# Kernel optimization log

Measured on AMD Instinct MI355X. Metric: run time of the kernel, lower is better.

## Reference

```python
import jax, jax.numpy as jnp
import numpy as np

N = 50000
EPS = 1e-5

def gcn_conv(x, W, b, edge_index):
    # PyG GCNConv: transform first, then normalized aggregation with self-loops
    xw = x @ W  # [N, out]
    src = jnp.concatenate([edge_index[0], jnp.arange(N)])  # add self-loops
    dst = jnp.concatenate([edge_index[1], jnp.arange(N)])
    deg = jax.ops.segment_sum(jnp.ones_like(dst, dtype=xw.dtype), dst, num_segments=N)
    dis = jnp.where(deg > 0, deg ** -0.5, 0.0)
    norm = dis[src] * dis[dst]  # [E+N]
    out = jax.ops.segment_sum(norm[:, None] * xw[src], dst, num_segments=N)
    return out + b

def batchnorm(x, gamma, beta):
    mean = x.mean(axis=0)
    var = ((x - mean) ** 2).mean(axis=0)  # biased var (training mode)
    return gamma * (x - mean) * jax.lax.rsqrt(var + EPS) + beta

def lrelu(x):
    return jnp.where(x > 0, x, 0.1 * x)

def setup_inputs() -> dict:
    key = jax.random.key(0)
    ks = jax.random.split(key, 12)
    E = 800000
    d = {
        "x": jax.random.normal(ks[0], (N, 3), dtype=jnp.float32),
        "edge_index": jax.random.randint(ks[1], (2, E), 0, N),
        "W1": jax.random.normal(ks[2], (3, 64), dtype=jnp.float32) * (1.0 / np.sqrt(3)),
        "b1": jnp.zeros((64,), jnp.float32),
        "g1": jnp.ones((64,), jnp.float32),
        "be1": jnp.zeros((64,), jnp.float32),
        "W2": jax.random.normal(ks[3], (64, 64), dtype=jnp.float32) * 0.125,
        "b2": jnp.zeros((64,), jnp.float32),
        "g2": jnp.ones((64,), jnp.float32),
        "be2": jnp.zeros((64,), jnp.float32),
        "W3": jax.random.normal(ks[4], (64, 256), dtype=jnp.float32) * 0.125,
        "b3": jnp.zeros((256,), jnp.float32),
        "g3": jnp.ones((256,), jnp.float32),
        "be3": jnp.zeros((256,), jnp.float32),
        "W4": jax.random.normal(ks[5], (256, 1), dtype=jnp.float32) * (1.0 / 16.0),
        "b4": jnp.zeros((1,), jnp.float32),
    }
    return d

def reference(x, edge_index, W1, b1, g1, be1, W2, b2, g2, be2, W3, b3, g3, be3, W4, b4):
    h = lrelu(batchnorm(gcn_conv(x, W1, b1, edge_index), g1, be1))
    h = lrelu(batchnorm(gcn_conv(h, W2, b2, edge_index), g2, be2))
    h = lrelu(batchnorm(gcn_conv(h, W3, b3, edge_index), g3, be3))
    h = gcn_conv(h, W4, b4, edge_index)
    return jax.nn.sigmoid(h)
```

## Files before the change

kernel.cpp:

```cpp
#include <hip/hip_runtime.h>
#include <math.h>

#define NN 50000
#define NP 50048
#define NB (NP / 64)
#define SCAN_NB ((NN + 255) / 256)
#define NBKT ((NN + 255) / 256)

typedef unsigned short u16;
typedef unsigned int u32;

typedef __bf16 bf16x8 __attribute__((ext_vector_type(8)));
typedef float f32x4 __attribute__((ext_vector_type(4)));

__device__ __forceinline__ u16 f2bf(float f) {
    u32 u = __float_as_uint(f);
    u32 r = (u + 0x7FFFu + ((u >> 16) & 1u)) >> 16;
    return (u16)r;
}
__device__ __forceinline__ float bf2f_lo(u32 v) { return __uint_as_float(v << 16); }
__device__ __forceinline__ float bf2f_hi(u32 v) { return __uint_as_float(v & 0xFFFF0000u); }

__global__ __launch_bounds__(256) void k_binA(const int* __restrict__ dst, int E,
                                              int* __restrict__ bcntT, int nblk) {
    __shared__ int h[NBKT];
    for (int i = threadIdx.x; i < NBKT; i += 256) h[i] = 0;
    __syncthreads();
    int base = blockIdx.x * 4096;
#pragma unroll
    for (int i = 0; i < 16; i++) {
        int e = base + i * 256 + threadIdx.x;
        if (e < E) atomicAdd(&h[dst[e] >> 8], 1);
    }
    __syncthreads();
    for (int i = threadIdx.x; i < NBKT; i += 256) bcntT[i * nblk + blockIdx.x] = h[i];
}

__global__ __launch_bounds__(256) void k_binT(const int* __restrict__ bcntT,
        int* __restrict__ colpre, int* __restrict__ tot, int nblk) {
    __shared__ int sh[256];
    int k = blockIdx.x, t = threadIdx.x;
    int v = (t < nblk) ? bcntT[k * nblk + t] : 0;
    sh[t] = v; __syncthreads();
    int inc = v;
    for (int o = 1; o < 256; o <<= 1) {
        int p = (t >= o) ? sh[t - o] : 0;
        __syncthreads();
        inc += p; sh[t] = inc;
        __syncthreads();
    }
    if (t < nblk) colpre[k * nblk + t] = inc - v;
    if (t == 255) tot[k] = inc;
}

__global__ __launch_bounds__(256) void k_scan_tot(const int* __restrict__ tot,
                                                  int* __restrict__ bstart, int E) {
    __shared__ int sh[256];
    int t = threadIdx.x;
    int v = (t < NBKT) ? tot[t] : 0;
    sh[t] = v; __syncthreads();
    int inc = v;
    for (int o = 1; o < 256; o <<= 1) {
        int p = (t >= o) ? sh[t - o] : 0;
        __syncthreads();
        inc += p; sh[t] = inc;
        __syncthreads();
    }
    if (t < NBKT) bstart[t] = inc - v;
    if (t == NBKT - 1) bstart[NBKT] = E;
}

__global__ __launch_bounds__(256) void k_binB(const int* __restrict__ src,
        const int* __restrict__ dst, int E, const int* __restrict__ bstart,
        const int* __restrict__ colpre, int nblk, u32* __restrict__ ebuf) {
    __shared__ int h[NBKT];
    __shared__ int base[NBKT];
    int b = blockIdx.x;
    for (int i = threadIdx.x; i < NBKT; i += 256) {
        h[i] = 0;
        base[i] = bstart[i] + colpre[i * nblk + b];
    }
    __syncthreads();
    int bb = b * 4096;
#pragma unroll
    for (int i = 0; i < 16; i++) {
        int e = bb + i * 256 + threadIdx.x;
        if (e < E) {
            int d = dst[e];
            int k = d >> 8;
            int r = atomicAdd(&h[k], 1);
            ebuf[base[k] + r] = ((u32)d << 16) | (u32)src[e];
        }
    }
}

__global__ __launch_bounds__(256) void k_bcnt_bsum_dis(const u32* __restrict__ ebuf,
        const int* __restrict__ bstart, int* __restrict__ cnt, float* __restrict__ dis,
        int* __restrict__ bsum, int n) {
    __shared__ int h[256];
    __shared__ int red[256];
    int k = blockIdx.x, t = threadIdx.x;
    h[t] = 0; __syncthreads();
    int beg = bstart[k], end = bstart[k + 1];
    for (int j = beg + t; j < end; j += 256)
        atomicAdd(&h[(ebuf[j] >> 16) & 255], 1);
    __syncthreads();
    int r = k * 256 + t;
    int d = h[t];
    bool valid = (r < n);
    if (valid) { cnt[r] = d; dis[r] = rsqrtf((float)d + 1.0f); }
    red[t] = valid ? d : 0;
    __syncthreads();
    for (int off = 128; off; off >>= 1) {
        if (t < off) red[t] += red[t + off];
        __syncthreads();
    }
    if (t == 0) bsum[k] = red[0];
}

__global__ void k_scan_bsum(int* __restrict__ bsum, int nb) {
    __shared__ int sh[256];
    int t = threadIdx.x;
    int v0 = (t < nb) ? bsum[t] : 0;
    sh[t] = v0; __syncthreads();
    int inc = v0;
    for (int off = 1; off < 256; off <<= 1) {
        int o = (t >= off) ? sh[t - off] : 0;
        __syncthreads();
        inc += o; sh[t] = inc;
        __syncthreads();
    }
    if (t < nb) bsum[t] = inc - v0;
}

__global__ __launch_bounds__(256) void k_sfpb(const int* __restrict__ cnt,
        const int* __restrict__ bpre, int* __restrict__ rowstart,
        const float* __restrict__ x, const float* __restrict__ dis,
        float* __restrict__ p0, const u32* __restrict__ ebuf,
        const int* __restrict__ bstart, u16* __restrict__ adj, int n, int E) {
    __shared__ int sh[256];
    __shared__ int cur[256];
    int b = blockIdx.x, t = threadIdx.x;
    int i = b * 256 + t;
    int v0 = (i < n) ? cnt[i] : 0;
    sh[t] = v0; __syncthreads();
    int inc = v0;
    for (int off = 1; off < 256; off <<= 1) {
        int o = (t >= off) ? sh[t - off] : 0;
        __syncthreads();
        inc += o; sh[t] = inc;
        __syncthreads();
    }
    int rs = bpre[b] + inc - v0;
    if (i < n) {
        rowstart[i] = rs;
        float dv = dis[i];
        ((float4*)p0)[i] = make_float4(dv * x[i * 3], dv * x[i * 3 + 1], dv * x[i * 3 + 2], 0.f);
    }
    if (b == gridDim.x - 1 && t == 0) rowstart[n] = E;
    cur[t] = rs;
    __syncthreads();
    int beg = bstart[b], end = bstart[b + 1];
    for (int j = beg + t; j < end; j += 256) {
        u32 e = ebuf[j];
        int p = atomicAdd(&cur[(e >> 16) & 255], 1);
        adj[p] = (u16)(e & 0xFFFF);
    }
}

__global__ void k_wprep_all(const float* __restrict__ W2, const float* __restrict__ W3,
                            u16* __restrict__ w2h, u16* __restrict__ w2l,
                            u16* __restrict__ w3h, u16* __restrict__ w3l) {
    int idx = blockIdx.x * 256 + threadIdx.x;
    float w; u16* ph; u16* pl; int slot;
    if (idx < 64 * 64) {
        int o = idx >> 6, k = idx & 63;
        w = W2[k * 64 + o]; ph = w2h; pl = w2l; slot = o * 64 + k;
    } else if (idx < 64 * 64 + 256 * 64) {
        int i2 = idx - 64 * 64;
        int o = i2 >> 6, k = i2 & 63;
        w = W3[k * 256 + o]; ph = w3h; pl = w3l; slot = o * 64 + k;
    } else return;
    u16 h = f2bf(w);
    float hf = __uint_as_float((u32)h << 16);
    ph[slot] = h;
    pl[slot] = f2bf(w - hf);
}

__global__ void k_gather3(const int* __restrict__ rowstart, const u16* __restrict__ adj,
                          const float* __restrict__ p0, const float* __restrict__ dis,
                          float* __restrict__ z, int n) {
    int row = blockIdx.x * 256 + threadIdx.x;
    if (row >= n) return;
    const float4* P4 = (const float4*)p0;
    float4 v = P4[row];
    float a0 = v.x, a1 = v.y, a2 = v.z;
    int beg = rowstart[row], end = rowstart[row + 1];
    for (int j = beg; j < end; j++) {
        int s = (int)__builtin_nontemporal_load(adj + j);
        float4 w = P4[s];
        a0 += w.x; a1 += w.y; a2 += w.z;
    }
    float dv = dis[row];
    z[row * 3] = dv * a0; z[row * 3 + 1] = dv * a1; z[row * 3 + 2] = dv * a2;
}

__global__ __launch_bounds__(256) void k_gather64_bf16(const int* __restrict__ rowstart,
        const u16* __restrict__ adj, const u16* __restrict__ pb,
        const float* __restrict__ dis, u16* __restrict__ zb, int n) {
    int row = blockIdx.x * 16 + (threadIdx.x >> 4);
    int lane = threadIdx.x & 15;
    if (row >= n) return;
    uint2 v = *((const uint2*)(pb + ((size_t)row << 6)) + lane);
    float a0 = bf2f_lo(v.x), a1 = bf2f_hi(v.x), a2 = bf2f_lo(v.y), a3 = bf2f_hi(v.y);
    int beg = rowstart[row], end = rowstart[row + 1];
    int j = beg;
    for (; j + 3 < end; j += 4) {
        int s0 = (int)__builtin_nontemporal_load(adj + j);
        int s1 = (int)__builtin_nontemporal_load(adj + j + 1);
        int s2 = (int)__builtin_nontemporal_load(adj + j + 2);
        int s3 = (int)__builtin_nontemporal_load(adj + j + 3);
        uint2 v0 = *((const uint2*)(pb + ((size_t)s0 << 6)) + lane);
        uint2 v1 = *((const uint2*)(pb + ((size_t)s1 << 6)) + lane);
        uint2 v2 = *((const uint2*)(pb + ((size_t)s2 << 6)) + lane);
        uint2 v3 = *((const uint2*)(pb + ((size_t)s3 << 6)) + lane);
        a0 += (bf2f_lo(v0.x) + bf2f_lo(v1.x)) + (bf2f_lo(v2.x) + bf2f_lo(v3.x));
        a1 += (bf2f_hi(v0.x) + bf2f_hi(v1.x)) + (bf2f_hi(v2.x) + bf2f_hi(v3.x));
        a2 += (bf2f_lo(v0.y) + bf2f_lo(v1.y)) + (bf2f_lo(v2.y) + bf2f_lo(v3.y));
        a3 += (bf2f_hi(v0.y) + bf2f_hi(v1.y)) + (bf2f_hi(v2.y) + bf2f_hi(v3.y));
    }
    for (; j < end; j++) {
        int s = (int)__builtin_nontemporal_load(adj + j);
        uint2 v0 = *((const uint2*)(pb + ((size_t)s << 6)) + lane);
        a0 += bf2f_lo(v0.x); a1 += bf2f_hi(v0.x);
        a2 += bf2f_lo(v0.y); a3 += bf2f_hi(v0.y);
    }
    float dv = dis[row];
    uint2 o;
    o.x = (u32)f2bf(a0 * dv) | ((u32)f2bf(a1 * dv) << 16);
    o.y = (u32)f2bf(a2 * dv) | ((u32)f2bf(a3 * dv) << 16);
    ((uint2*)(zb + ((size_t)row << 6)))[lane] = o;
}

__global__ void k_gather1_final(const int* __restrict__ rowstart, const u16* __restrict__ adj,
                                const float* __restrict__ q, const float* __restrict__ dis,
                                const float* __restrict__ b4, float* __restrict__ out, int n) {
    int row = blockIdx.x * 256 + threadIdx.x;
    if (row >= n) return;
    float acc = q[row];
    int beg = rowstart[row], end = rowstart[row + 1];
    for (int j = beg; j < end; j++)
        acc += q[(int)__builtin_nontemporal_load(adj + j)];
    float v = dis[row] * acc + b4[0];
    out[row] = 1.f / (1.f + expf(-v));
}

__global__ __launch_bounds__(256) void k_mgemm(const u16* __restrict__ zb,
        const u16* __restrict__ wth, const u16* __restrict__ wtl,
        u16* __restrict__ t, int tstride,
        double* __restrict__ pS, double* __restrict__ pQ) {
    const int wv = threadIdx.x >> 6, lane = threadIdx.x & 63;
    const int lc = lane & 15, lk = lane >> 4;
    const int r0 = blockIdx.x * 64;
    const int col = blockIdx.y * 64 + wv * 16 + lc;

    const bf16x8* wh = (const bf16x8*)(wth + (size_t)col * 64 + lk * 8);
    const bf16x8* wl = (const bf16x8*)(wtl + (size_t)col * 64 + lk * 8);
    bf16x8 bh0 = wh[0], bh1 = wh[4];
    bf16x8 bl0 = wl[0], bl1 = wl[4];

    f32x4 acc[4] = {};
#pragma unroll
    for (int rt = 0; rt < 4; rt++) {
        const bf16x8* ap = (const bf16x8*)(zb + (size_t)(r0 + rt * 16 + lc) * 64 + lk * 8);
        bf16x8 a0 = ap[0], a1 = ap[4];
        acc[rt] = __builtin_amdgcn_mfma_f32_16x16x32_bf16(a0, bh0, acc[rt], 0, 0, 0);
        acc[rt] = __builtin_amdgcn_mfma_f32_16x16x32_bf16(a1, bh1, acc[rt], 0, 0, 0);
        acc[rt] = __builtin_amdgcn_mfma_f32_16x16x32_bf16(a0, bl0, acc[rt], 0, 0, 0);
        acc[rt] = __builtin_amdgcn_mfma_f32_16x16x32_bf16(a1, bl1, acc[rt], 0, 0, 0);
    }
#pragma unroll
    for (int rt = 0; rt < 4; rt++) {
        int rowb = r0 + rt * 16 + lk * 4;
#pragma unroll
        for (int rg = 0; rg < 4; rg++)
            t[(size_t)(rowb + rg) * tstride + col] = f2bf(acc[rt][rg]);
    }
    float s = 0.f, q = 0.f;
#pragma unroll
    for (int rt = 0; rt < 4; rt++)
#pragma unroll
        for (int rg = 0; rg < 4; rg++) { float v = acc[rt][rg]; s += v; q += v * v; }
    s += __shfl_xor(s, 16); q += __shfl_xor(q, 16);
    s += __shfl_xor(s, 32); q += __shfl_xor(q, 32);
    if (lane < 16) {
        pS[(size_t)col * NB + blockIdx.x] = (double)s;
        pQ[(size_t)col * NB + blockIdx.x] = (double)q;
    }
}

__global__ __launch_bounds__(256) void k_gemm3_stats(const float* __restrict__ z,
        const float* __restrict__ W, u16* __restrict__ t,
        double* __restrict__ pS, double* __restrict__ pQ, int n) {
    __shared__ float sH[64 * 4];
    __shared__ float sW[3 * 64];
    __shared__ double red[2 * 16 * 64];
    const int tid = threadIdx.x;
    const int r0 = blockIdx.x * 64;
    for (int i = tid; i < 192; i += 256) {
        int r = i / 3, c = i - r * 3;
        sH[r * 4 + c] = (r0 + r < n) ? z[(size_t)(r0 + r) * 3 + c] : 0.f;
    }
    if (tid < 48) ((float4*)sW)[tid] = ((const float4*)W)[tid];
    __syncthreads();
    const int tx = tid & 15, ty = tid >> 4;
    float4 acc[4];
#pragma unroll
    for (int r = 0; r < 4; r++) acc[r] = make_float4(0.f, 0.f, 0.f, 0.f);
    const float4* sW4 = (const float4*)sW;
#pragma unroll
    for (int k = 0; k < 3; k++) {
        float4 wv = sW4[k * 16 + tx];
#pragma unroll
        for (int r = 0; r < 4; r++) {
            float hs = sH[(ty * 4 + r) * 4 + k];
            acc[r].x += hs * wv.x; acc[r].y += hs * wv.y;
            acc[r].z += hs * wv.z; acc[r].w += hs * wv.w;
        }
    }
#pragma unroll
    for (int r = 0; r < 4; r++) {
        int row = r0 + ty * 4 + r;
        if (row < n) {
            uint2 o;
            o.x = (u32)f2bf(acc[r].x) | ((u32)f2bf(acc[r].y) << 16);
            o.y = (u32)f2bf(acc[r].z) | ((u32)f2bf(acc[r].w) << 16);
            *(uint2*)&t[(size_t)row * 64 + tx * 4] = o;
        }
    }
    double* redS = red;
    double* redQ = red + 16 * 64;
    double s0 = 0, s1 = 0, s2 = 0, s3 = 0, q0 = 0, q1 = 0, q2 = 0, q3 = 0;
#pragma unroll
    for (int r = 0; r < 4; r++) {
        s0 += acc[r].x; q0 += (double)acc[r].x * acc[r].x;
        s1 += acc[r].y; q1 += (double)acc[r].y * acc[r].y;
        s2 += acc[r].z; q2 += (double)acc[r].z * acc[r].z;
        s3 += acc[r].w; q3 += (double)acc[r].w * acc[r].w;
    }
    int base = ty * 64 + tx * 4;
    redS[base + 0] = s0; redS[base + 1] = s1; redS[base + 2] = s2; redS[base + 3] = s3;
    redQ[base + 0] = q0; redQ[base + 1] = q1; redQ[base + 2] = q2; redQ[base + 3] = q3;
    __syncthreads();
    if (ty == 0) {
#pragma unroll
        for (int jj = 0; jj < 4; jj++) {
            int c = tx * 4 + jj;
            double S = 0, Q = 0;
            for (int g = 0; g < 16; g++) { S += redS[g * 64 + c]; Q += redQ[g * 64 + c]; }
            pS[(size_t)c * NB + blockIdx.x] = S;
            pQ[(size_t)c * NB + blockIdx.x] = Q;
        }
    }
}

template<int F>
__global__ __launch_bounds__(256) void k_stats_fin(const double* __restrict__ pS,
        const double* __restrict__ pQ, const float* __restrict__ g,
        const float* __restrict__ be, double* __restrict__ st, int n) {
    __shared__ double shS[256], shQ[256];
    int c = blockIdx.x, t = threadIdx.x;
    double s = 0, q = 0;
    for (int i = t; i < NB; i += 256) {
        s += pS[(size_t)c * NB + i];
        q += pQ[(size_t)c * NB + i];
    }
    shS[t] = s; shQ[t] = q;
    __syncthreads();
    for (int off = 128; off; off >>= 1) {
        if (t < off) { shS[t] += shS[t + off]; shQ[t] += shQ[t + off]; }
        __syncthreads();
    }
    if (t == 0) {
        double mean = shS[0] / n;
        double var = shQ[0] / n - mean * mean;
        if (var < 0.0) var = 0.0;
        double mult = (double)g[c] / sqrt(var + 1e-5);
        st[2 * F + c] = mult;
        st[3 * F + c] = (double)be[c] - mult * mean;
    }
}

__global__ void k_apply64(const u16* __restrict__ t, const float* __restrict__ dis,
                          const double* __restrict__ st, u16* __restrict__ p, int n) {
    int idx = blockIdx.x * 256 + threadIdx.x;
    if (idx >= n * 16) return;
    int row = idx >> 4, c = (idx & 15) * 4;
    uint2 v = ((const uint2*)t)[idx];
    float f0 = bf2f_lo(v.x), f1 = bf2f_hi(v.x), f2 = bf2f_lo(v.y), f3 = bf2f_hi(v.y);
    float m0 = (float)st[128 + c], m1 = (float)st[129 + c],
          m2 = (float)st[130 + c], m3 = (float)st[131 + c];
    float a0 = (float)st[192 + c], a1 = (float)st[193 + c],
          a2 = (float)st[194 + c], a3 = (float)st[195 + c];
    float r0 = m0 * f0 + a0; r0 = r0 > 0.f ? r0 : 0.1f * r0;
    float r1 = m1 * f1 + a1; r1 = r1 > 0.f ? r1 : 0.1f * r1;
    float r2 = m2 * f2 + a2; r2 = r2 > 0.f ? r2 : 0.1f * r2;
    float r3 = m3 * f3 + a3; r3 = r3 > 0.f ? r3 : 0.1f * r3;
    float dv = dis[row];
    uint2 o;
    o.x = (u32)f2bf(r0 * dv) | ((u32)f2bf(r1 * dv) << 16);
    o.y = (u32)f2bf(r2 * dv) | ((u32)f2bf(r3 * dv) << 16);
    ((uint2*)p)[idx] = o;
}

__global__ void k_apply3_dot(const u16* __restrict__ t, const double* __restrict__ st,
                             const float* __restrict__ dis, const float* __restrict__ W4,
                             float* __restrict__ q, int n) {
    int row = blockIdx.x * 4 + (threadIdx.x >> 6);
    int lane = threadIdx.x & 63;
    if (row >= n) return;
    uint2 v = ((const uint2*)t)[(size_t)row * 64 + lane];
    float f0 = bf2f_lo(v.x), f1 = bf2f_hi(v.x), f2 = bf2f_lo(v.y), f3 = bf2f_hi(v.y);
    int c = lane * 4;
    float m0 = (float)st[512 + c], m1 = (float)st[513 + c],
          m2 = (float)st[514 + c], m3 = (float)st[515 + c];
    float a0 = (float)st[768 + c], a1 = (float)st[769 + c],
          a2 = (float)st[770 + c], a3 = (float)st[771 + c];
    float b0 = m0 * f0 + a0; b0 = b0 > 0.f ? b0 : 0.1f * b0;
    float b1 = m1 * f1 + a1; b1 = b1 > 0.f ? b1 : 0.1f * b1;
    float b2 = m2 * f2 + a2; b2 = b2 > 0.f ? b2 : 0.1f * b2;
    float b3 = m3 * f3 + a3; b3 = b3 > 0.f ? b3 : 0.1f * b3;
    float4 w = ((const float4*)W4)[lane];
    float s = b0 * w.x + b1 * w.y + b2 * w.z + b3 * w.w;
#pragma unroll
    for (int off = 32; off; off >>= 1) s += __shfl_down(s, off);
    if (lane == 0) q[row] = dis[row] * s;
}

extern "C" void kernel_launch(void* const* d_in, const int* in_sizes, int n_in,
                              void* d_out, int out_size, void* d_ws, size_t ws_size,
                              hipStream_t stream) {
    const float* x  = (const float*)d_in[0];
    const int*   ei = (const int*)d_in[1];
    const int E = in_sizes[1] / 2;
    const int* src = ei;
    const int* dst = ei + E;
    const float* W1 = (const float*)d_in[2];
    const float* g1 = (const float*)d_in[4];
    const float* be1= (const float*)d_in[5];
    const float* W2 = (const float*)d_in[6];
    const float* g2 = (const float*)d_in[8];
    const float* be2= (const float*)d_in[9];
    const float* W3 = (const float*)d_in[10];
    const float* g3 = (const float*)d_in[12];
    const float* be3= (const float*)d_in[13];
    const float* W4 = (const float*)d_in[14];
    const float* b4 = (const float*)d_in[15];
    float* out = (float*)d_out;

    const int nblk = (E + 4095) / 4096;

    u16*   T    = (u16*)d_ws;
    u16*   P    = T + (size_t)NP * 256;
    u16*   Zb   = P + (size_t)NN * 64;
    u16*   Wt2h = Zb + (size_t)NP * 64;
    u16*   Wt2l = Wt2h + 64 * 64;
    u16*   Wt3h = Wt2l + 64 * 64;
    u16*   Wt3l = Wt3h + 256 * 64;
    double* st  = (double*)(Wt3l + 256 * 64);
    double *st0 = st, *st1 = st + 1024, *st2 = st + 2048;
    double* pS  = st + 3 * 1024;
    double* pQ  = pS + (size_t)256 * NB;
    float* Z3   = (float*)(pQ + (size_t)256 * NB);
    float* P0   = Z3 + NN * 3;
    float* Q    = P0 + NN * 4;
    float* dis  = Q + NN;
    int* cnt      = (int*)(dis + NN);
    int* rowstart = cnt + NN;
    u16* adj      = (u16*)(rowstart + NN + 8);
    int* bsum     = (int*)(adj + E + (E & 1));
    u32* ebuf     = (u32*)(bsum + SCAN_NB + 4);
    int* bcntT    = (int*)(ebuf + E);
    int* colpre   = bcntT + NBKT * nblk;
    int* tot      = colpre + NBKT * nblk;
    int* bstart   = tot + NBKT + 4;

    hipMemsetAsync(Zb + (size_t)NN * 64, 0, (size_t)(NP - NN) * 64 * sizeof(u16), stream);

    k_binA<<<nblk, 256, 0, stream>>>(dst, E, bcntT, nblk);
    k_binT<<<NBKT, 256, 0, stream>>>(bcntT, colpre, tot, nblk);
    k_scan_tot<<<1, 256, 0, stream>>>(tot, bstart, E);
    k_binB<<<nblk, 256, 0, stream>>>(src, dst, E, bstart, colpre, nblk, ebuf);
    k_bcnt_bsum_dis<<<NBKT, 256, 0, stream>>>(ebuf, bstart, cnt, dis, bsum, NN);
    k_scan_bsum<<<1, 256, 0, stream>>>(bsum, SCAN_NB);
    k_sfpb<<<SCAN_NB, 256, 0, stream>>>(cnt, bsum, rowstart, x, dis, P0, ebuf, bstart,
                                        adj, NN, E);
    k_wprep_all<<<(64 * 64 + 256 * 64 + 255) / 256, 256, 0, stream>>>(W2, W3, Wt2h, Wt2l, Wt3h, Wt3l);

    const int rows_grid = (NN + 255) / 256;
    const int g16_grid  = (NN + 15) / 16;
    const int wave4_grid = (NN + 3) / 4;
    const int app_grid = (NN * 16 + 255) / 256;

    k_gather3<<<rows_grid, 256, 0, stream>>>(rowstart, adj, P0, dis, Z3, NN);
    k_gemm3_stats<<<NB, 256, 0, stream>>>(Z3, W1, T, pS, pQ, NN);
    k_stats_fin<64><<<64, 256, 0, stream>>>(pS, pQ, g1, be1, st0, NN);
    k_apply64<<<app_grid, 256, 0, stream>>>(T, dis, st0, P, NN);

    k_gather64_bf16<<<g16_grid, 256, 0, stream>>>(rowstart, adj, P, dis, Zb, NN);
    k_mgemm<<<dim3(NB, 1), 256, 0, stream>>>(Zb, Wt2h, Wt2l, T, 64, pS, pQ);
    k_stats_fin<64><<<64, 256, 0, stream>>>(pS, pQ, g2, be2, st1, NN);
    k_apply64<<<app_grid, 256, 0, stream>>>(T, dis, st1, P, NN);

    k_gather64_bf16<<<g16_grid, 256, 0, stream>>>(rowstart, adj, P, dis, Zb, NN);
    k_mgemm<<<dim3(NB, 4), 256, 0, stream>>>(Zb, Wt3h, Wt3l, T, 256, pS, pQ);
    k_stats_fin<256><<<256, 256, 0, stream>>>(pS, pQ, g3, be3, st2, NN);

    k_apply3_dot<<<wave4_grid, 256, 0, stream>>>(T, st2, dis, W4, Q, NN);
    k_gather1_final<<<rows_grid, 256, 0, stream>>>(rowstart, adj, Q, dis, b4, out, NN);
}
```

Baseline: 195.0 us.

## Fuse batchnorm+leaky-relu apply into neighbor gather and merge weight prep into binning

Removes the separate apply kernels. The gather kernel now reads raw pre-BN bf16 features and applies the BN affine transform, leaky ReLU and source-degree scaling to each neighbor on the fly. The weight-prep kernel is folded into extra blocks of the first binning kernel to save a launch. This drops a full write and read of the intermediate P array and two launches, but repeats the BN and activation work once per edge and adds a dis[s] load for every neighbor.

New measurement: 189.7 us. -2.7%, faster.

```diff
diff --git a/kernel.cpp b/kernel.cpp
--- a/kernel.cpp
+++ b/kernel.cpp
@@ -21,8 +21,28 @@
 __device__ __forceinline__ float bf2f_lo(u32 v) { return __uint_as_float(v << 16); }
 __device__ __forceinline__ float bf2f_hi(u32 v) { return __uint_as_float(v & 0xFFFF0000u); }
 
-__global__ __launch_bounds__(256) void k_binA(const int* __restrict__ dst, int E,
-                                              int* __restrict__ bcntT, int nblk) {
+__global__ __launch_bounds__(256) void k_binA_wprep(const int* __restrict__ dst, int E,
+        int* __restrict__ bcntT, int nblk,
+        const float* __restrict__ W2, const float* __restrict__ W3,
+        u16* __restrict__ w2h, u16* __restrict__ w2l,
+        u16* __restrict__ w3h, u16* __restrict__ w3l) {
+    if (blockIdx.x >= (unsigned)nblk) {
+        int idx = (blockIdx.x - nblk) * 256 + threadIdx.x;
+        float w; u16* ph; u16* pl; int slot;
+        if (idx < 64 * 64) {
+            int o = idx >> 6, k = idx & 63;
+            w = W2[k * 64 + o]; ph = w2h; pl = w2l; slot = o * 64 + k;
+        } else if (idx < 64 * 64 + 256 * 64) {
+            int i2 = idx - 64 * 64;
+            int o = i2 >> 6, k = i2 & 63;
+            w = W3[k * 256 + o]; ph = w3h; pl = w3l; slot = o * 64 + k;
+        } else return;
+        u16 h = f2bf(w);
+        float hf = __uint_as_float((u32)h << 16);
+        ph[slot] = h;
+        pl[slot] = f2bf(w - hf);
+        return;
+    }
     __shared__ int h[NBKT];
     for (int i = threadIdx.x; i < NBKT; i += 256) h[i] = 0;
     __syncthreads();
@@ -168,25 +188,6 @@
     }
 }
 
-__global__ void k_wprep_all(const float* __restrict__ W2, const float* __restrict__ W3,
-                            u16* __restrict__ w2h, u16* __restrict__ w2l,
-                            u16* __restrict__ w3h, u16* __restrict__ w3l) {
-    int idx = blockIdx.x * 256 + threadIdx.x;
-    float w; u16* ph; u16* pl; int slot;
-    if (idx < 64 * 64) {
-        int o = idx >> 6, k = idx & 63;
-        w = W2[k * 64 + o]; ph = w2h; pl = w2l; slot = o * 64 + k;
-    } else if (idx < 64 * 64 + 256 * 64) {
-        int i2 = idx - 64 * 64;
-        int o = i2 >> 6, k = i2 & 63;
-        w = W3[k * 256 + o]; ph = w3h; pl = w3l; slot = o * 64 + k;
-    } else return;
-    u16 h = f2bf(w);
-    float hf = __uint_as_float((u32)h << 16);
-    ph[slot] = h;
-    pl[slot] = f2bf(w - hf);
-}
-
 __global__ void k_gather3(const int* __restrict__ rowstart, const u16* __restrict__ adj,
                           const float* __restrict__ p0, const float* __restrict__ dis,
                           float* __restrict__ z, int n) {
@@ -205,14 +206,28 @@
     z[row * 3] = dv * a0; z[row * 3 + 1] = dv * a1; z[row * 3 + 2] = dv * a2;
 }
 
-__global__ __launch_bounds__(256) void k_gather64_bf16(const int* __restrict__ rowstart,
-        const u16* __restrict__ adj, const u16* __restrict__ pb,
-        const float* __restrict__ dis, u16* __restrict__ zb, int n) {
+__global__ __launch_bounds__(256) void k_gather64_bn(const int* __restrict__ rowstart,
+        const u16* __restrict__ adj, const u16* __restrict__ tb,
+        const float* __restrict__ dis, const double* __restrict__ st,
+        u16* __restrict__ zb, int n) {
     int row = blockIdx.x * 16 + (threadIdx.x >> 4);
     int lane = threadIdx.x & 15;
     if (row >= n) return;
-    uint2 v = *((const uint2*)(pb + ((size_t)row << 6)) + lane);
-    float a0 = bf2f_lo(v.x), a1 = bf2f_hi(v.x), a2 = bf2f_lo(v.y), a3 = bf2f_hi(v.y);
+    int c = lane * 4;
+    const float m0 = (float)st[128 + c], m1 = (float)st[129 + c],
+                m2 = (float)st[130 + c], m3 = (float)st[131 + c];
+    const float b0 = (float)st[192 + c], b1 = (float)st[193 + c],
+                b2 = (float)st[194 + c], b3 = (float)st[195 + c];
+    float a0, a1, a2, a3;
+    {
+        uint2 v = *((const uint2*)(tb + ((size_t)row << 6)) + lane);
+        float ds = dis[row];
+        float r0 = m0 * bf2f_lo(v.x) + b0; r0 = r0 > 0.f ? r0 : 0.1f * r0;
+        float r1 = m1 * bf2f_hi(v.x) + b1; r1 = r1 > 0.f ? r1 : 0.1f * r1;
+        float r2 = m2 * bf2f_lo(v.y) + b2; r2 = r2 > 0.f ? r2 : 0.1f * r2;
+        float r3 = m3 * bf2f_hi(v.y) + b3; r3 = r3 > 0.f ? r3 : 0.1f * r3;
+        a0 = r0 * ds; a1 = r1 * ds; a2 = r2 * ds; a3 = r3 * ds;
+    }
     int beg = rowstart[row], end = rowstart[row + 1];
     int j = beg;
     for (; j + 3 < end; j += 4) {
@@ -220,20 +235,38 @@
         int s1 = (int)__builtin_nontemporal_load(adj + j + 1);
         int s2 = (int)__builtin_nontemporal_load(adj + j + 2);
         int s3 = (int)__builtin_nontemporal_load(adj + j + 3);
-        uint2 v0 = *((const uint2*)(pb + ((size_t)s0 << 6)) + lane);
-        uint2 v1 = *((const uint2*)(pb + ((size_t)s1 << 6)) + lane);
-        uint2 v2 = *((const uint2*)(pb + ((size_t)s2 << 6)) + lane);
-        uint2 v3 = *((const uint2*)(pb + ((size_t)s3 << 6)) + lane);
-        a0 += (bf2f_lo(v0.x) + bf2f_lo(v1.x)) + (bf2f_lo(v2.x) + bf2f_lo(v3.x));
-        a1 += (bf2f_hi(v0.x) + bf2f_hi(v1.x)) + (bf2f_hi(v2.x) + bf2f_hi(v3.x));
-        a2 += (bf2f_lo(v0.y) + bf2f_lo(v1.y)) + (bf2f_lo(v2.y) + bf2f_lo(v3.y));
-        a3 += (bf2f_hi(v0.y) + bf2f_hi(v1.y)) + (bf2f_hi(v2.y) + bf2f_hi(v3.y));
+        uint2 v0 = *((const uint2*)(tb + ((size_t)s0 << 6)) + lane);
+        uint2 v1 = *((const uint2*)(tb + ((size_t)s1 << 6)) + lane);
+        uint2 v2 = *((const uint2*)(tb + ((size_t)s2 << 6)) + lane);
+        uint2 v3 = *((const uint2*)(tb + ((size_t)s3 << 6)) + lane);
+        float d0 = dis[s0], d1 = dis[s1], d2 = dis[s2], d3 = dis[s3];
+        float r;
+        r = m0 * bf2f_lo(v0.x) + b0; r = r > 0.f ? r : 0.1f * r; a0 += r * d0;
+        r = m1 * bf2f_hi(v0.x) + b1; r = r > 0.f ? r : 0.1f * r; a1 += r * d0;
+        r = m2 * bf2f_lo(v0.y) + b2; r = r > 0.f ? r : 0.1f * r; a2 += r * d0;
+        r = m3 * bf2f_hi(v0.y) + b3; r = r > 0.f ? r : 0.1f * r; a3 += r * d0;
+        r = m0 * bf2f_lo(v1.x) + b0; r = r > 0.f ? r : 0.1f * r; a0 += r * d1;
+        r = m1 * bf2f_hi(v1.x) + b1; r = r > 0.f ? r : 0.1f * r; a1 += r * d1;
+        r = m2 * bf2f_lo(v1.y) + b2; r = r > 0.f ? r : 0.1f * r; a2 += r * d1;
+        r = m3 * bf2f_hi(v1.y) + b3; r = r > 0.f ? r : 0.1f * r; a3 += r * d1;
+        r = m0 * bf2f_lo(v2.x) + b0; r = r > 0.f ? r : 0.1f * r; a0 += r * d2;
+        r = m1 * bf2f_hi(v2.x) + b1; r = r > 0.f ? r : 0.1f * r; a1 += r * d2;
+        r = m2 * bf2f_lo(v2.y) + b2; r = r > 0.f ? r : 0.1f * r; a2 += r * d2;
+        r = m3 * bf2f_hi(v2.y) + b3; r = r > 0.f ? r : 0.1f * r; a3 += r * d2;
+        r = m0 * bf2f_lo(v3.x) + b0; r = r > 0.f ? r : 0.1f * r; a0 += r * d3;
+        r = m1 * bf2f_hi(v3.x) + b1; r = r > 0.f ? r : 0.1f * r; a1 += r * d3;
+        r = m2 * bf2f_lo(v3.y) + b2; r = r > 0.f ? r : 0.1f * r; a2 += r * d3;
+        r = m3 * bf2f_hi(v3.y) + b3; r = r > 0.f ? r : 0.1f * r; a3 += r * d3;
     }
     for (; j < end; j++) {
         int s = (int)__builtin_nontemporal_load(adj + j);
-        uint2 v0 = *((const uint2*)(pb + ((size_t)s << 6)) + lane);
-        a0 += bf2f_lo(v0.x); a1 += bf2f_hi(v0.x);
-        a2 += bf2f_lo(v0.y); a3 += bf2f_hi(v0.y);
+        uint2 v0 = *((const uint2*)(tb + ((size_t)s << 6)) + lane);
+        float ds = dis[s];
+        float r;
+        r = m0 * bf2f_lo(v0.x) + b0; r = r > 0.f ? r : 0.1f * r; a0 += r * ds;
+        r = m1 * bf2f_hi(v0.x) + b1; r = r > 0.f ? r : 0.1f * r; a1 += r * ds;
+        r = m2 * bf2f_lo(v0.y) + b2; r = r > 0.f ? r : 0.1f * r; a2 += r * ds;
+        r = m3 * bf2f_hi(v0.y) + b3; r = r > 0.f ? r : 0.1f * r; a3 += r * ds;
     }
     float dv = dis[row];
     uint2 o;
@@ -389,28 +422,6 @@
         st[2 * F + c] = mult;
         st[3 * F + c] = (double)be[c] - mult * mean;
     }
-}
-
-__global__ void k_apply64(const u16* __restrict__ t, const float* __restrict__ dis,
-                          const double* __restrict__ st, u16* __restrict__ p, int n) {
-    int idx = blockIdx.x * 256 + threadIdx.x;
-    if (idx >= n * 16) return;
-    int row = idx >> 4, c = (idx & 15) * 4;
-    uint2 v = ((const uint2*)t)[idx];
-    float f0 = bf2f_lo(v.x), f1 = bf2f_hi(v.x), f2 = bf2f_lo(v.y), f3 = bf2f_hi(v.y);
-    float m0 = (float)st[128 + c], m1 = (float)st[129 + c],
-          m2 = (float)st[130 + c], m3 = (float)st[131 + c];
-    float a0 = (float)st[192 + c], a1 = (float)st[193 + c],
-          a2 = (float)st[194 + c], a3 = (float)st[195 + c];
-    float r0 = m0 * f0 + a0; r0 = r0 > 0.f ? r0 : 0.1f * r0;
-    float r1 = m1 * f1 + a1; r1 = r1 > 0.f ? r1 : 0.1f * r1;
-    float r2 = m2 * f2 + a2; r2 = r2 > 0.f ? r2 : 0.1f * r2;
-    float r3 = m3 * f3 + a3; r3 = r3 > 0.f ? r3 : 0.1f * r3;
-    float dv = dis[row];
-    uint2 o;
-    o.x = (u32)f2bf(r0 * dv) | ((u32)f2bf(r1 * dv) << 16);
-    o.y = (u32)f2bf(r2 * dv) | ((u32)f2bf(r3 * dv) << 16);
-    ((uint2*)p)[idx] = o;
 }
 
 __global__ void k_apply3_dot(const u16* __restrict__ t, const double* __restrict__ st,
@@ -461,8 +472,7 @@
     const int nblk = (E + 4095) / 4096;
 
     u16*   T    = (u16*)d_ws;
-    u16*   P    = T + (size_t)NP * 256;
-    u16*   Zb   = P + (size_t)NN * 64;
+    u16*   Zb   = T + (size_t)NP * 256;
     u16*   Wt2h = Zb + (size_t)NP * 64;
     u16*   Wt2l = Wt2h + 64 * 64;
     u16*   Wt3h = Wt2l + 64 * 64;
@@ -487,7 +497,8 @@
 
     hipMemsetAsync(Zb + (size_t)NN * 64, 0, (size_t)(NP - NN) * 64 * sizeof(u16), stream);
 
-    k_binA<<<nblk, 256, 0, stream>>>(dst, E, bcntT, nblk);
+    k_binA_wprep<<<nblk + 80, 256, 0, stream>>>(dst, E, bcntT, nblk,
+                                                W2, W3, Wt2h, Wt2l, Wt3h, Wt3l);
     k_binT<<<NBKT, 256, 0, stream>>>(bcntT, colpre, tot, nblk);
     k_scan_tot<<<1, 256, 0, stream>>>(tot, bstart, E);
     k_binB<<<nblk, 256, 0, stream>>>(src, dst, E, bstart, colpre, nblk, ebuf);
@@ -495,24 +506,20 @@
     k_scan_bsum<<<1, 256, 0, stream>>>(bsum, SCAN_NB);
     k_sfpb<<<SCAN_NB, 256, 0, stream>>>(cnt, bsum, rowstart, x, dis, P0, ebuf, bstart,
                                         adj, NN, E);
-    k_wprep_all<<<(64 * 64 + 256 * 64 + 255) / 256, 256, 0, stream>>>(W2, W3, Wt2h, Wt2l, Wt3h, Wt3l);
 
     const int rows_grid = (NN + 255) / 256;
     const int g16_grid  = (NN + 15) / 16;
     const int wave4_grid = (NN + 3) / 4;
-    const int app_grid = (NN * 16 + 255) / 256;
 
     k_gather3<<<rows_grid, 256, 0, stream>>>(rowstart, adj, P0, dis, Z3, NN);
     k_gemm3_stats<<<NB, 256, 0, stream>>>(Z3, W1, T, pS, pQ, NN);
     k_stats_fin<64><<<64, 256, 0, stream>>>(pS, pQ, g1, be1, st0, NN);
-    k_apply64<<<app_grid, 256, 0, stream>>>(T, dis, st0, P, NN);
-
-    k_gather64_bf16<<<g16_grid, 256, 0, stream>>>(rowstart, adj, P, dis, Zb, NN);
+
+    k_gather64_bn<<<g16_grid, 256, 0, stream>>>(rowstart, adj, T, dis, st0, Zb, NN);
     k_mgemm<<<dim3(NB, 1), 256, 0, stream>>>(Zb, Wt2h, Wt2l, T, 64, pS, pQ);
     k_stats_fin<64><<<64, 256, 0, stream>>>(pS, pQ, g2, be2, st1, NN);
-    k_apply64<<<app_grid, 256, 0, stream>>>(T, dis, st1, P, NN);
-
-    k_gather64_bf16<<<g16_grid, 256, 0, stream>>>(rowstart, adj, P, dis, Zb, NN);
+
+    k_gather64_bn<<<g16_grid, 256, 0, stream>>>(rowstart, adj, T, dis, st1, Zb, NN);
     k_mgemm<<<dim3(NB, 4), 256, 0, stream>>>(Zb, Wt3h, Wt3l, T, 256, pS, pQ);
     k_stats_fin<256><<<256, 256, 0, stream>>>(pS, pQ, g3, be3, st2, NN);
 
```
